# Kernel tuning notes

Hardware: AMD Instinct MI355X
Metric: run time of the kernel (lower is better)

Reference implementation:

```python
import jax, jax.numpy as jnp
import numpy as np

N_NODES = 50000
N_EDGES = 800000
D_S, D_R, D_E, D_X, D_P, NUM_CLASSES = 64, 16, 64, 16, 64, 10


def setup_inputs() -> dict:
    key = jax.random.key(0)
    ks = jax.random.split(key, 11)
    return {
        "O": jax.random.normal(ks[0], (N_NODES, D_S), dtype=jnp.float32),
        "X": jax.random.normal(ks[1], (N_NODES, D_X), dtype=jnp.float32),
        "R_a": jax.random.normal(ks[2], (N_EDGES, D_R), dtype=jnp.float32),
        "senders": jax.random.randint(ks[3], (N_EDGES,), 0, N_NODES, dtype=jnp.int32).astype(jnp.int64),
        "receivers": jax.random.randint(ks[4], (N_EDGES,), 0, N_NODES, dtype=jnp.int32).astype(jnp.int64),
        "W_r": jax.random.normal(ks[5], (2 * D_S + D_R, D_E), dtype=jnp.float32) * 0.05,
        "b_r": jax.random.normal(ks[6], (D_E,), dtype=jnp.float32) * 0.05,
        "W_o": jax.random.normal(ks[7], (D_S + D_X + D_E, D_P), dtype=jnp.float32) * 0.05,
        "b_o": jax.random.normal(ks[8], (D_P,), dtype=jnp.float32) * 0.05,
        "W_s": jax.random.normal(ks[9], (D_P, NUM_CLASSES), dtype=jnp.float32) * 0.05,
        "b_s": jax.random.normal(ks[10], (NUM_CLASSES,), dtype=jnp.float32) * 0.05,
    }


def reference(O, X, R_a, senders, receivers, W_r, b_r, W_o, b_o, W_s, b_s):
    n_nodes = O.shape[0]
    # marshalling: gather sender/receiver node states, concat relation attrs -> [E, 2*D_S + D_R]
    B = jnp.concatenate([O[senders], O[receivers], R_a], axis=-1)
    # relation model phi_r: per-edge effects [E, D_E]
    E = B @ W_r + b_r
    # scatter-aggregate edge effects onto receiver nodes -> [N, D_E]
    E_hat = jax.ops.segment_sum(E, receivers, num_segments=n_nodes)
    # object model phi_o on concat(state, external, aggregated effects)
    C = jnp.concatenate([O, X, E_hat], axis=-1)
    P = C @ W_o + b_o
    scores = P @ W_s + b_s
    probs = jax.nn.softmax(scores, axis=1)
    return probs
```

## Files before the change

### kernel.cpp

```cpp
#include <hip/hip_runtime.h>

#define N_NODES 50000
#define N_EDGES 800000

#define WS_A       ((size_t)0)
#define WS_COUNT   ((size_t)16384)
#define WS_CURSOR  ((size_t)216384)
#define WS_OFF     ((size_t)217088)
#define WS_RANK    ((size_t)417792)
#define WS_US      ((size_t)3618816)
#define WS_U01     ((size_t)6019072)
#define WS_WSORT   ((size_t)10019328)

#define NB_PRE   10
#define NB_CR    ((N_EDGES / 4 + 255) / 256)
#define NB_ALLOC ((N_NODES + 255) / 256)
#define NB_NU    ((N_NODES * 5 + 255) / 256)

__device__ __forceinline__ unsigned int f32_to_bf16_rne(float f) {
    unsigned int x = __float_as_uint(f);
    return (x + 0x7fffu + ((x >> 16) & 1u)) >> 16;
}

__global__ __launch_bounds__(256) void fused_prep_kernel(
    const float* __restrict__ W_r, const float* __restrict__ b_r,
    const float* __restrict__ W_o, const float* __restrict__ b_o,
    const float* __restrict__ W_s, const float* __restrict__ b_s,
    const int* __restrict__ receivers,
    float* __restrict__ A, int* __restrict__ count, int* __restrict__ rank)
{
    __shared__ float Wc2[640];
    const int t = threadIdx.x;

    if (blockIdx.x < NB_PRE) {
        for (int idx = t; idx < 640; idx += 256) {
            const int row = 80 + idx / 10, c = idx % 10;
            float acc = 0.f;
            for (int j = 0; j < 64; ++j)
                acc = fmaf(W_o[row * 64 + j], W_s[j * 10 + c], acc);
            Wc2[idx] = acc;
        }
        __syncthreads();

        for (int g = blockIdx.x * 256 + t; g < 3616; g += NB_PRE * 256) {
            if (g < 1356) {
                const int row = g / 6, c = 10 + g % 6;
                A[row * 16 + c] = 0.f;
            } else if (g < 2156) {
                const int i = g - 1356, row = i / 10, c = i % 10;
                float acc = 0.f;
                for (int j = 0; j < 64; ++j)
                    acc = fmaf(W_o[row * 64 + j], W_s[j * 10 + c], acc);
                A[row * 16 + c] = acc;
            } else if (g < 3596) {
                const int i = g - 2156, k = i / 10, c = i % 10;
                const int wrow = (k < 64) ? k : (k < 80 ? 128 + (k - 64) : 64 + (k - 80));
                const int arow = (k < 64) ? 80 + k : (k < 80 ? 144 + (k - 64) : 160 + (k - 80));
                const float* src = W_r + (size_t)wrow * 64;
                float acc = 0.f;
                for (int m = 0; m < 64; ++m)
                    acc = fmaf(src[m], Wc2[m * 10 + c], acc);
                A[arow * 16 + c] = acc;
            } else if (g < 3606) {
                const int c = g - 3596;
                float acc = 0.f;
                for (int m = 0; m < 64; ++m)
                    acc = fmaf(b_r[m], Wc2[m * 10 + c], acc);
                A[224 * 16 + c] = acc;
            } else {
                const int c = g - 3606;
                float acc = b_s[c];
                for (int j = 0; j < 64; ++j)
                    acc = fmaf(b_o[j], W_s[j * 10 + c], acc);
                A[225 * 16 + c] = acc;
            }
        }
    } else {
        const int bt = (blockIdx.x - NB_PRE) * 256 + t;
        if (bt * 4 >= N_EDGES) return;
        const int4 r4 = reinterpret_cast<const int4*>(receivers)[bt];
        int4 k4;
        k4.x = atomicAdd(count + r4.x, 1);
        k4.y = atomicAdd(count + r4.y, 1);
        k4.z = atomicAdd(count + r4.z, 1);
        k4.w = atomicAdd(count + r4.w, 1);
        reinterpret_cast<int4*>(rank)[bt] = k4;
    }
}

__global__ __launch_bounds__(256) void fused_mid_kernel(
    const float* __restrict__ O, const float* __restrict__ X,
    const float* __restrict__ A,
    const int* __restrict__ count, unsigned int* __restrict__ cursor,
    int* __restrict__ off,
    float* __restrict__ us, float* __restrict__ u01)
{
    __shared__ float2 lA[226 * 5];
    const int t = threadIdx.x;

    if (blockIdx.x < NB_ALLOC) {
        const int n = blockIdx.x * 256 + t;
        const int lane = t & 63;
        const int c = (n < N_NODES) ? count[n] : 0;

        int pre = c;
#pragma unroll
        for (int d = 1; d < 64; d <<= 1) {
            const int v = __shfl_up(pre, d);
            if (lane >= d) pre += v;
        }
        const int total = __shfl(pre, 63);
        int base = 0;
        if (lane == 63) base = (int)atomicAdd(cursor, (unsigned int)total);
        base = __shfl(base, 63);

        if (n < N_NODES) off[n] = base + pre - c;
    } else {
        for (int i = t; i < 226 * 5; i += 256) {
            const int row = i / 5, cp = i - row * 5;
            lA[i] = *reinterpret_cast<const float2*>(A + (size_t)row * 16 + 2 * cp);
        }
        __syncthreads();

        const int tid = (blockIdx.x - NB_ALLOC) * 256 + t;
        if (tid >= N_NODES * 5) return;
        const int n = tid / 5;
        const int cp = tid - n * 5;

        float vs0 = 0.f, vs1 = 0.f, v00 = 0.f, v01 = 0.f, v10 = 0.f, v11 = 0.f;

        const float4* Ov = reinterpret_cast<const float4*>(O + (size_t)n * 64);
#pragma unroll
        for (int kc = 0; kc < 16; ++kc) {
            const float4 o4 = Ov[kc];
#pragma unroll
            for (int j = 0; j < 4; ++j) {
                const float ov = (j == 0) ? o4.x : (j == 1) ? o4.y : (j == 2) ? o4.z : o4.w;
                const int k = kc * 4 + j;
                const float2 aO = lA[k * 5 + cp];
                const float2 aS = lA[(80 + k) * 5 + cp];
                const float2 aD = lA[(160 + k) * 5 + cp];
                v00 = fmaf(ov, aO.x, v00); v01 = fmaf(ov, aO.y, v01);
                vs0 = fmaf(ov, aS.x, vs0); vs1 = fmaf(ov, aS.y, vs1);
                v10 = fmaf(ov, aD.x, v10); v11 = fmaf(ov, aD.y, v11);
            }
        }
        const float4* Xv = reinterpret_cast<const float4*>(X + (size_t)n * 16);
#pragma unroll
        for (int kc = 0; kc < 4; ++kc) {
            const float4 x4 = Xv[kc];
#pragma unroll
            for (int j = 0; j < 4; ++j) {
                const float xv = (j == 0) ? x4.x : (j == 1) ? x4.y : (j == 2) ? x4.z : x4.w;
                const int k = 64 + kc * 4 + j;
                const float2 aX = lA[k * 5 + cp];
                v00 = fmaf(xv, aX.x, v00); v01 = fmaf(xv, aX.y, v01);
            }
        }

        const float2 c0 = lA[224 * 5 + cp];
        const float2 c1 = lA[225 * 5 + cp];
        *reinterpret_cast<float2*>(us + (size_t)n * 12 + 2 * cp) = make_float2(vs0, vs1);
        *reinterpret_cast<float2*>(u01 + (size_t)n * 20 + 2 * cp) =
            make_float2(v00 + c1.x, v01 + c1.y);
        *reinterpret_cast<float2*>(u01 + (size_t)n * 20 + 10 + 2 * cp) =
            make_float2(v10 + c0.x, v11 + c0.y);
    }
}

__global__ __launch_bounds__(256) void edge_w_kernel(
    const float* __restrict__ R_a,
    const int* __restrict__ senders, const int* __restrict__ receivers,
    const int* __restrict__ rank, const int* __restrict__ off,
    const float* __restrict__ us, const float* __restrict__ A,
    unsigned int* __restrict__ wsort)
{
    const int e = blockIdx.x * blockDim.x + threadIdx.x;
    if (e >= N_EDGES) return;
    const int s = senders[e];
    const int r = receivers[e];
    const int pos = off[r] + rank[e];

    const float4* U = reinterpret_cast<const float4*>(us + (size_t)s * 12);
    const float4 ua = U[0];
    const float4 ub = U[1];
    const float4 uc = U[2];
    float a[10] = {ua.x, ua.y, ua.z, ua.w, ub.x, ub.y, ub.z, ub.w, uc.x, uc.y};

    const float4* Rv = reinterpret_cast<const float4*>(R_a + (size_t)e * 16);
#pragma unroll
    for (int kc = 0; kc < 4; ++kc) {
        const float4 b4 = Rv[kc];
        const float* A0 = A + (size_t)(144 + kc * 4) * 16;
#pragma unroll
        for (int c = 0; c < 10; ++c) a[c] = fmaf(b4.x, A0[c], a[c]);
#pragma unroll
        for (int c = 0; c < 10; ++c) a[c] = fmaf(b4.y, A0[16 + c], a[c]);
#pragma unroll
        for (int c = 0; c < 10; ++c) a[c] = fmaf(b4.z, A0[32 + c], a[c]);
#pragma unroll
        for (int c = 0; c < 10; ++c) a[c] = fmaf(b4.w, A0[48 + c], a[c]);
    }

    unsigned int* wp = wsort + (size_t)pos * 5;
    wp[0] = f32_to_bf16_rne(a[0]) | (f32_to_bf16_rne(a[1]) << 16);
    wp[1] = f32_to_bf16_rne(a[2]) | (f32_to_bf16_rne(a[3]) << 16);
    wp[2] = f32_to_bf16_rne(a[4]) | (f32_to_bf16_rne(a[5]) << 16);
    wp[3] = f32_to_bf16_rne(a[6]) | (f32_to_bf16_rne(a[7]) << 16);
    wp[4] = f32_to_bf16_rne(a[8]) | (f32_to_bf16_rne(a[9]) << 16);
}

#define CH_REC 512

__global__ __launch_bounds__(256) void node_score_kernel(
    const float* __restrict__ u01,
    const int* __restrict__ off, const int* __restrict__ count,
    const unsigned int* __restrict__ w,
    float* __restrict__ out)
{
    __shared__ unsigned int lw[CH_REC * 5];
    const int t = threadIdx.x;
    const int n0 = blockIdx.x * 16;
    const int g = t >> 4;
    const int lane = t & 15;
    const int n = n0 + g;

    const int beg16 = off[n0];
    const int end16 = off[n0 + 15] + count[n0 + 15];

    const int beg = off[n];
    const int cnt = count[n];
    const int dge = cnt;

    const int cc = (lane < 10) ? lane : 0;
    const int half = cc >> 1;
    const int sh = (cc & 1) * 16;

    float sc = u01[(size_t)n * 20 + cc] + (float)dge * u01[(size_t)n * 20 + 10 + cc];

    for (int c0 = beg16; c0 < end16; c0 += CH_REC) {
        const int nrec = min(CH_REC, end16 - c0);
        const int ndw = nrec * 5;
        __syncthreads();
        for (int i = t; i < ndw; i += 256)
            lw[i] = w[(size_t)c0 * 5 + i];
        __syncthreads();

        const int j0 = max(beg, c0);
        const int j1 = min(beg + cnt, c0 + nrec);
        for (int j = j0; j < j1; ++j) {
            const unsigned int v = lw[(j - c0) * 5 + half];
            sc += __uint_as_float((v >> sh) << 16);
        }
    }

    float m = (lane < 10) ? sc : -3.0e38f;
#pragma unroll
    for (int d = 1; d < 16; d <<= 1) m = fmaxf(m, __shfl_xor(m, d, 16));
    const float ex = (lane < 10) ? __expf(sc - m) : 0.f;
    float sum = ex;
#pragma unroll
    for (int d = 1; d < 16; d <<= 1) sum += __shfl_xor(sum, d, 16);
    if (lane < 10) out[(size_t)n * 10 + lane] = ex / sum;
}

extern "C" void kernel_launch(void* const* d_in, const int* in_sizes, int n_in,
                              void* d_out, int out_size, void* d_ws, size_t ws_size,
                              hipStream_t stream)
{
    const float* O    = (const float*)d_in[0];
    const float* X    = (const float*)d_in[1];
    const float* R_a  = (const float*)d_in[2];
    const int* senders   = (const int*)d_in[3];
    const int* receivers = (const int*)d_in[4];
    const float* W_r  = (const float*)d_in[5];
    const float* b_r  = (const float*)d_in[6];
    const float* W_o  = (const float*)d_in[7];
    const float* b_o  = (const float*)d_in[8];
    const float* W_s  = (const float*)d_in[9];
    const float* b_s  = (const float*)d_in[10];
    float* out = (float*)d_out;
    char* ws = (char*)d_ws;

    float* A      = (float*)(ws + WS_A);
    int* count    = (int*)(ws + WS_COUNT);
    unsigned int* cursor = (unsigned int*)(ws + WS_CURSOR);
    int* off      = (int*)(ws + WS_OFF);
    int* rank     = (int*)(ws + WS_RANK);
    float* us     = (float*)(ws + WS_US);
    float* u01    = (float*)(ws + WS_U01);
    unsigned int* wsort = (unsigned int*)(ws + WS_WSORT);

    hipMemsetAsync(count, 0, (size_t)(200000 + 4 + 384), stream);

    fused_prep_kernel<<<NB_PRE + NB_CR, 256, 0, stream>>>(
        W_r, b_r, W_o, b_o, W_s, b_s, receivers, A, count, rank);

    fused_mid_kernel<<<NB_ALLOC + NB_NU, 256, 0, stream>>>(
        O, X, A, count, cursor, off, us, u01);

    edge_w_kernel<<<(N_EDGES + 255) / 256, 256, 0, stream>>>(
        R_a, senders, receivers, rank, off, us, A, wsort);

    node_score_kernel<<<N_NODES / 16, 256, 0, stream>>>(
        u01, off, count, wsort, out);
}
```

Before: 116.8 us.

## Privatize receiver counters into eight groups and store per-edge ranks as bytes

After: 119.3 us. 2.1% more time.

```diff
diff --git a/kernel.cpp b/kernel.cpp
--- a/kernel.cpp
+++ b/kernel.cpp
@@ -5,12 +5,13 @@
 
 #define WS_A       ((size_t)0)
 #define WS_COUNT   ((size_t)16384)
-#define WS_CURSOR  ((size_t)216384)
 #define WS_OFF     ((size_t)217088)
-#define WS_RANK    ((size_t)417792)
-#define WS_US      ((size_t)3618816)
-#define WS_U01     ((size_t)6019072)
-#define WS_WSORT   ((size_t)10019328)
+#define WS_RANK8   ((size_t)417792)
+#define WS_CURSOR  ((size_t)1220544)
+#define WS_CPRIV   ((size_t)1220608)
+#define WS_US      ((size_t)2824192)
+#define WS_U01     ((size_t)5226496)
+#define WS_WSORT   ((size_t)9228288)
 
 #define NB_PRE   10
 #define NB_CR    ((N_EDGES / 4 + 255) / 256)
@@ -27,7 +28,8 @@
     const float* __restrict__ W_o, const float* __restrict__ b_o,
     const float* __restrict__ W_s, const float* __restrict__ b_s,
     const int* __restrict__ receivers,
-    float* __restrict__ A, int* __restrict__ count, int* __restrict__ rank)
+    float* __restrict__ A, int* __restrict__ cpriv,
+    unsigned char* __restrict__ rank8)
 {
     __shared__ float Wc2[640];
     const int t = threadIdx.x;
@@ -76,23 +78,25 @@
             }
         }
     } else {
-        const int bt = (blockIdx.x - NB_PRE) * 256 + t;
-        if (bt * 4 >= N_EDGES) return;
-        const int4 r4 = reinterpret_cast<const int4*>(receivers)[bt];
-        int4 k4;
-        k4.x = atomicAdd(count + r4.x, 1);
-        k4.y = atomicAdd(count + r4.y, 1);
-        k4.z = atomicAdd(count + r4.z, 1);
-        k4.w = atomicAdd(count + r4.w, 1);
-        reinterpret_cast<int4*>(rank)[bt] = k4;
+        const int bt = blockIdx.x - NB_PRE;
+        int* cp = cpriv + (size_t)(bt & 7) * N_NODES;
+        const int t4 = bt * 256 + t;
+        if (t4 * 4 >= N_EDGES) return;
+        const int4 r4 = reinterpret_cast<const int4*>(receivers)[t4];
+        uchar4 k4;
+        k4.x = (unsigned char)atomicAdd(cp + r4.x, 1);
+        k4.y = (unsigned char)atomicAdd(cp + r4.y, 1);
+        k4.z = (unsigned char)atomicAdd(cp + r4.z, 1);
+        k4.w = (unsigned char)atomicAdd(cp + r4.w, 1);
+        reinterpret_cast<uchar4*>(rank8)[t4] = k4;
     }
 }
 
 __global__ __launch_bounds__(256) void fused_mid_kernel(
     const float* __restrict__ O, const float* __restrict__ X,
     const float* __restrict__ A,
-    const int* __restrict__ count, unsigned int* __restrict__ cursor,
-    int* __restrict__ off,
+    int* __restrict__ cpriv, int* __restrict__ count,
+    unsigned int* __restrict__ cursor, int* __restrict__ off,
     float* __restrict__ us, float* __restrict__ u01)
 {
     __shared__ float2 lA[226 * 5];
@@ -101,7 +105,18 @@
     if (blockIdx.x < NB_ALLOC) {
         const int n = blockIdx.x * 256 + t;
         const int lane = t & 63;
-        const int c = (n < N_NODES) ? count[n] : 0;
+        int c = 0;
+        if (n < N_NODES) {
+            int run = 0;
+#pragma unroll
+            for (int g = 0; g < 8; ++g) {
+                const int v = cpriv[(size_t)g * N_NODES + n];
+                cpriv[(size_t)g * N_NODES + n] = run;
+                run += v;
+            }
+            c = run;
+            count[n] = c;
+        }
 
         int pre = c;
 #pragma unroll
@@ -171,7 +186,8 @@
 __global__ __launch_bounds__(256) void edge_w_kernel(
     const float* __restrict__ R_a,
     const int* __restrict__ senders, const int* __restrict__ receivers,
-    const int* __restrict__ rank, const int* __restrict__ off,
+    const unsigned char* __restrict__ rank8, const int* __restrict__ off,
+    const int* __restrict__ goff,
     const float* __restrict__ us, const float* __restrict__ A,
     unsigned int* __restrict__ wsort)
 {
@@ -179,7 +195,8 @@
     if (e >= N_EDGES) return;
     const int s = senders[e];
     const int r = receivers[e];
-    const int pos = off[r] + rank[e];
+    const int g = (e >> 10) & 7;
+    const int pos = off[r] + goff[(size_t)g * N_NODES + r] + (int)rank8[e];
 
     const float4* U = reinterpret_cast<const float4*>(us + (size_t)s * 12);
     const float4 ua = U[0];
@@ -284,23 +301,24 @@
 
     float* A      = (float*)(ws + WS_A);
     int* count    = (int*)(ws + WS_COUNT);
+    int* off      = (int*)(ws + WS_OFF);
+    unsigned char* rank8 = (unsigned char*)(ws + WS_RANK8);
     unsigned int* cursor = (unsigned int*)(ws + WS_CURSOR);
-    int* off      = (int*)(ws + WS_OFF);
-    int* rank     = (int*)(ws + WS_RANK);
+    int* cpriv    = (int*)(ws + WS_CPRIV);
     float* us     = (float*)(ws + WS_US);
     float* u01    = (float*)(ws + WS_U01);
     unsigned int* wsort = (unsigned int*)(ws + WS_WSORT);
 
-    hipMemsetAsync(count, 0, (size_t)(200000 + 4 + 384), stream);
+    hipMemsetAsync(ws + WS_CURSOR, 0, (size_t)(64 + 8 * N_NODES * 4), stream);
 
     fused_prep_kernel<<<NB_PRE + NB_CR, 256, 0, stream>>>(
-        W_r, b_r, W_o, b_o, W_s, b_s, receivers, A, count, rank);
+        W_r, b_r, W_o, b_o, W_s, b_s, receivers, A, cpriv, rank8);
 
     fused_mid_kernel<<<NB_ALLOC + NB_NU, 256, 0, stream>>>(
-        O, X, A, count, cursor, off, us, u01);
+        O, X, A, cpriv, count, cursor, off, us, u01);
 
     edge_w_kernel<<<(N_EDGES + 255) / 256, 256, 0, stream>>>(
-        R_a, senders, receivers, rank, off, us, A, wsort);
+        R_a, senders, receivers, rank8, off, cpriv, us, A, wsort);
 
     node_score_kernel<<<N_NODES / 16, 256, 0, stream>>>(
         u01, off, count, wsort, out);
```
